# Kernel tuning notes

Measured on AMD Instinct MI355X. Metric: run time of the kernel, lower is better.

## Reference

```python
import jax, jax.numpy as jnp
import numpy as np

ALPHA = 0.2  # LeakyReLU negative slope
NEG_INF = -9e15  # matches torch's -9000000000000000.0


def setup_inputs() -> dict:
    key = jax.random.key(0)
    k1, k2, k3, k4 = jax.random.split(key, 4)
    B, T, N, F_in, D = 4, 32, 512, 128, 128
    h = jax.random.normal(k1, (B, T, N, F_in), dtype=jnp.float32)
    adj = jax.random.randint(k2, (N, N), 0, 2, dtype=jnp.int32)
    # params: W ~ Linear(in_dim, out_dim, bias=False); a ~ Linear(2*out_dim, 1, bias=False)
    W = jax.random.normal(k3, (F_in, D), dtype=jnp.float32) * 0.05
    a = jax.random.normal(k4, (2 * D,), dtype=jnp.float32) * 0.05
    return {"h": h, "adj": adj, "W": W, "a": a}


def reference(h, adj, W, a):
    # h: (B,T,N,F_in), adj: (N,N), W: (F_in,D), a: (2D,)
    D = W.shape[1]
    Wh = jnp.einsum('btnf,fd->btnd', h, W)  # (B,T,N,D)
    # a . [Wh_i ; Wh_j] == a_src . Wh_i + a_dst . Wh_j -- avoids (N,N,2D) concat
    a_src, a_dst = a[:D], a[D:]
    e_src = Wh @ a_src  # (B,T,N)
    e_dst = Wh @ a_dst  # (B,T,N)
    e = jax.nn.leaky_relu(e_src[..., :, None] + e_dst[..., None, :], ALPHA)  # (B,T,N,N)
    e = jnp.where(adj > 0, e, jnp.float32(NEG_INF))
    attention = jax.nn.softmax(e, axis=-1)  # dropout is identity at eval
    h_prime = jnp.einsum('btij,btjd->btid', attention, Wh)  # (B,T,N,D)
    return h_prime
```

## Files before the change

kernel.cpp:

```cpp
#include <hip/hip_runtime.h>
#include <math.h>

typedef __attribute__((ext_vector_type(8))) short bf16x8;
typedef __attribute__((ext_vector_type(4))) float f32x4;

#define MFMA(a, b, c) __builtin_amdgcn_mfma_f32_16x16x32_bf16(a, b, c, 0, 0, 0)

constexpr int GN = 128;
constexpr int NN = 512;
constexpr int FD = 128;
#define LOG2E 1.4426950408889634f

__device__ inline unsigned rne_top16(float x) {
    unsigned u = __float_as_uint(x);
    return u + 0x7fffu + ((u >> 16) & 1u);
}
__device__ inline unsigned pack_top16(unsigned e1, unsigned e0) {
    return __builtin_amdgcn_perm(e1, e0, 0x07060302u);
}

__global__ __launch_bounds__(512, 2) void gat_fused_kernel(
    const float* __restrict__ h, const float* __restrict__ a,
    const int* __restrict__ adj, const float* __restrict__ W,
    float* __restrict__ out)
{
    __shared__ __attribute__((aligned(16))) unsigned short sWh[65536];
    __shared__ __attribute__((aligned(16))) unsigned short sWc[8192];
    __shared__ __attribute__((aligned(16))) float sEsrc[NN];
    __shared__ __attribute__((aligned(16))) float sEdst[NN];

    const int bid = blockIdx.x;
    const int xcd = bid & 7, slot = bid >> 3;
    const int g  = xcd * 16 + (slot >> 1);
    const int hf = slot & 1;
    const int t = threadIdx.x, lane = t & 63, w = t >> 6;
    const int l15 = lane & 15, q8 = (lane >> 4) * 8;
    const float* hg = h + (size_t)g * NN * FD;

    f32x4 acc1[4][8];
    #pragma unroll
    for (int mt = 0; mt < 4; ++mt)
        #pragma unroll
        for (int nb = 0; nb < 8; ++nb) acc1[mt][nb] = (f32x4){0.f, 0.f, 0.f, 0.f};

    const int sd = w * 16 + l15;

    #pragma unroll
    for (int kk = 0; kk < 4; ++kk) {
        float4 hv[8];
        #pragma unroll
        for (int mt = 0; mt < 4; ++mt) {
            const float* src = hg + (size_t)(w * 64 + mt * 16 + l15) * FD
                             + kk * 32 + q8;
            hv[2 * mt]     = *(const float4*)src;
            hv[2 * mt + 1] = *(const float4*)(src + 4);
        }

        if (kk > 0) __syncthreads();
        {
            const int kbase = kk * 32 + q8;
            unsigned hi[8], lo[8];
            #pragma unroll
            for (int idx = 0; idx < 8; ++idx) {
                const float wv = W[(kbase + idx) * FD + sd];
                const unsigned u = __float_as_uint(wv);
                hi[idx] = u;
                lo[idx] = rne_top16(wv - __uint_as_float(u & 0xffff0000u));
            }
            uint4 H4, L4;
            H4.x = pack_top16(hi[1], hi[0]); H4.y = pack_top16(hi[3], hi[2]);
            H4.z = pack_top16(hi[5], hi[4]); H4.w = pack_top16(hi[7], hi[6]);
            L4.x = pack_top16(lo[1], lo[0]); L4.y = pack_top16(lo[3], lo[2]);
            L4.z = pack_top16(lo[5], lo[4]); L4.w = pack_top16(lo[7], lo[6]);
            *(uint4*)&sWc[t * 8]        = H4;
            *(uint4*)&sWc[4096 + t * 8] = L4;
        }
        __syncthreads();

        bf16x8 ah[4], al[4];
        #pragma unroll
        for (int mt = 0; mt < 4; ++mt) {
            const float4 f0 = hv[2 * mt], f1 = hv[2 * mt + 1];
            const float xs[8] = {f0.x, f0.y, f0.z, f0.w, f1.x, f1.y, f1.z, f1.w};
            union { bf16x8 v; unsigned u[4]; } H, L;
            #pragma unroll
            for (int j = 0; j < 4; ++j) {
                const unsigned e0 = __float_as_uint(xs[2 * j]);
                const unsigned e1 = __float_as_uint(xs[2 * j + 1]);
                H.u[j] = pack_top16(e1, e0);
                const unsigned l0 = rne_top16(xs[2*j]   - __uint_as_float(e0 & 0xffff0000u));
                const unsigned l1 = rne_top16(xs[2*j+1] - __uint_as_float(e1 & 0xffff0000u));
                L.u[j] = pack_top16(l1, l0);
            }
            ah[mt] = H.v; al[mt] = L.v;
        }
        #pragma unroll
        for (int nb = 0; nb < 8; ++nb) {
            const bf16x8 bh = *(const bf16x8*)&sWc[(nb * 64 + lane) * 8];
            const bf16x8 bl = *(const bf16x8*)&sWc[4096 + (nb * 64 + lane) * 8];
            #pragma unroll
            for (int mt = 0; mt < 4; ++mt) {
                acc1[mt][nb] = MFMA(al[mt], bh, acc1[mt][nb]);
                acc1[mt][nb] = MFMA(ah[mt], bl, acc1[mt][nb]);
                acc1[mt][nb] = MFMA(ah[mt], bh, acc1[mt][nb]);
            }
        }
    }

    {
        float av[8], bv[8];
        #pragma unroll
        for (int nb = 0; nb < 8; ++nb) {
            av[nb] = a[nb * 16 + l15];
            bv[nb] = a[FD + nb * 16 + l15];
        }
        #pragma unroll
        for (int mt = 0; mt < 4; ++mt)
            #pragma unroll
            for (int r = 0; r < 4; ++r) {
                float ps = 0.f, pd = 0.f;
                #pragma unroll
                for (int nb = 0; nb < 8; ++nb) {
                    ps += acc1[mt][nb][r] * av[nb];
                    pd += acc1[mt][nb][r] * bv[nb];
                }
                #pragma unroll
                for (int off = 1; off <= 8; off <<= 1) {
                    ps += __shfl_xor(ps, off);
                    pd += __shfl_xor(pd, off);
                }
                if (l15 == 0) {
                    const int row = w * 64 + mt * 16 + (lane >> 4) * 4 + r;
                    sEsrc[row] = ps * LOG2E;
                    sEdst[row] = pd * LOG2E;
                }
            }
    }

    {
        const int ib = 4 * ((lane >> 4) & 1);
        #pragma unroll
        for (int mt = 0; mt < 4; ++mt) {
            const int KK = w * 2 + (mt >> 1);
            const int lp2 = l15 + 16 * ((mt & 1) * 2 + (lane >> 5));
            #pragma unroll
            for (int nb = 0; nb < 8; ++nb) {
                const int off = ((KK * 8 + nb) * 64 + lp2) * 8 + ib;
                const unsigned r0 = rne_top16(acc1[mt][nb][0]);
                const unsigned r1 = rne_top16(acc1[mt][nb][1]);
                const unsigned r2 = rne_top16(acc1[mt][nb][2]);
                const unsigned r3 = rne_top16(acc1[mt][nb][3]);
                *(uint2*)&sWh[off] = make_uint2(pack_top16(r1, r0), pack_top16(r3, r2));
            }
        }
    }
    __syncthreads();

    const int rloc0 = w * 32 + l15;
    const int irow0 = hf * 256 + rloc0;
    const int irow1 = irow0 + 16;
    const float s0 = sEsrc[irow0];
    const float s1 = sEsrc[irow1];
    const int* adjr0 = adj + (size_t)irow0 * NN;
    const int* adjr1 = adj + (size_t)irow1 * NN;

    union { bf16x8 v; unsigned short s[8]; } bo;
    {
        const unsigned short oneb = (l15 == 0) ? (unsigned short)0x3f80 : (unsigned short)0;
        #pragma unroll
        for (int j = 0; j < 8; ++j) bo.s[j] = oneb;
    }

    f32x4 acc[2][8];
    #pragma unroll
    for (int mt = 0; mt < 2; ++mt)
        #pragma unroll
        for (int nb = 0; nb < 8; ++nb) acc[mt][nb] = (f32x4){0.f, 0.f, 0.f, 0.f};
    f32x4 accS0 = (f32x4){0.f, 0.f, 0.f, 0.f};
    f32x4 accS1 = (f32x4){0.f, 0.f, 0.f, 0.f};

    int4 n00 = *(const int4*)&adjr0[q8];
    int4 n01 = *(const int4*)&adjr0[q8 + 4];
    int4 n10 = *(const int4*)&adjr1[q8];
    int4 n11 = *(const int4*)&adjr1[q8 + 4];

    for (int KK = 0; KK < 16; ++KK) {
        const int4 m00 = n00, m01 = n01, m10 = n10, m11 = n11;
        if (KK < 15) {
            const int jb = (KK + 1) * 32 + q8;
            n00 = *(const int4*)&adjr0[jb];
            n01 = *(const int4*)&adjr0[jb + 4];
            n10 = *(const int4*)&adjr1[jb];
            n11 = *(const int4*)&adjr1[jb + 4];
        }
        const float* ep = &sEdst[KK * 32 + q8];
        const float4 ed0 = *(const float4*)ep;
        const float4 ed1 = *(const float4*)(ep + 4);
        const float ev[8] = {ed0.x, ed0.y, ed0.z, ed0.w, ed1.x, ed1.y, ed1.z, ed1.w};
        int ma0[8], ma1[8];
        *(int4*)&ma0[0] = m00; *(int4*)&ma0[4] = m01;
        *(int4*)&ma1[0] = m10; *(int4*)&ma1[4] = m11;

        union { bf16x8 v; unsigned u[4]; } H0, H1;
        unsigned uh0[8], uh1[8];
        #pragma unroll
        for (int i = 0; i < 8; ++i) {
            const float z0 = s0 + ev[i];
            float p0 = __builtin_amdgcn_exp2f(fmaxf(z0, 0.2f * z0));
            p0 = (ma0[i] > 0) ? p0 : 0.f;
            uh0[i] = __float_as_uint(p0);
            const float z1 = s1 + ev[i];
            float p1 = __builtin_amdgcn_exp2f(fmaxf(z1, 0.2f * z1));
            p1 = (ma1[i] > 0) ? p1 : 0.f;
            uh1[i] = __float_as_uint(p1);
        }
        #pragma unroll
        for (int j = 0; j < 4; ++j) {
            H0.u[j] = pack_top16(uh0[2*j+1], uh0[2*j]);
            H1.u[j] = pack_top16(uh1[2*j+1], uh1[2*j]);
        }
        #pragma unroll
        for (int nb = 0; nb < 8; ++nb) {
            const bf16x8 bh = *(const bf16x8*)&sWh[((KK * 8 + nb) * 64 + lane) * 8];
            acc[0][nb] = MFMA(H0.v, bh, acc[0][nb]);
            acc[1][nb] = MFMA(H1.v, bh, acc[1][nb]);
        }
        accS0 = MFMA(H0.v, bo.v, accS0);
        accS1 = MFMA(H1.v, bo.v, accS1);
    }

    #pragma unroll
    for (int r = 0; r < 4; ++r) {
        const float rl0 = 1.0f / __shfl(accS0[r], lane & 48);
        const float rl1 = 1.0f / __shfl(accS1[r], lane & 48);
        const int row0 = g * NN + hf * 256 + w * 32 + (lane >> 4) * 4 + r;
        const int row1 = row0 + 16;
        #pragma unroll
        for (int nb = 0; nb < 8; ++nb) {
            out[row0 * FD + nb * 16 + l15] = acc[0][nb][r] * rl0;
            out[row1 * FD + nb * 16 + l15] = acc[1][nb][r] * rl1;
        }
    }
}

extern "C" void kernel_launch(void* const* d_in, const int* in_sizes, int n_in,
                              void* d_out, int out_size, void* d_ws, size_t ws_size,
                              hipStream_t stream) {
    const float* h   = (const float*)d_in[0];
    const int*   adj = (const int*)d_in[1];
    const float* W   = (const float*)d_in[2];
    const float* a   = (const float*)d_in[3];
    float* out = (float*)d_out;
    (void)d_ws; (void)ws_size;

    gat_fused_kernel<<<256, 512, 0, stream>>>(h, a, adj, W, out);
}
```

Measured before the change: 117.4 us.

## Double block to 1024 threads, split attention K-range across wave pairs

Launches 1024-thread blocks (16 waves) instead of 512. Each wave now computes 32 rows of Wh instead of 64, and W is converted to split bf16 once into the (not yet used) upper half of sWh instead of being restaged per k-slice, which removes the per-slice barriers. In the attention phase, pairs of waves split the 16 key chunks in half, and partial outputs and row sums are reduced through shared memory before the normalised store. This adds two barriers and an LDS reduction, and at 1024 threads each wave has a smaller register budget, in exchange for more waves per CU to hide latency.

```diff
diff --git a/kernel.cpp b/kernel.cpp
--- a/kernel.cpp
+++ b/kernel.cpp
@@ -19,13 +19,12 @@
     return __builtin_amdgcn_perm(e1, e0, 0x07060302u);
 }
 
-__global__ __launch_bounds__(512, 2) void gat_fused_kernel(
+__global__ __launch_bounds__(1024) void gat_fused_kernel(
     const float* __restrict__ h, const float* __restrict__ a,
     const int* __restrict__ adj, const float* __restrict__ W,
     float* __restrict__ out)
 {
     __shared__ __attribute__((aligned(16))) unsigned short sWh[65536];
-    __shared__ __attribute__((aligned(16))) unsigned short sWc[8192];
     __shared__ __attribute__((aligned(16))) float sEsrc[NN];
     __shared__ __attribute__((aligned(16))) float sEdst[NN];
 
@@ -37,49 +36,49 @@
     const int l15 = lane & 15, q8 = (lane >> 4) * 8;
     const float* hg = h + (size_t)g * NN * FD;
 
-    f32x4 acc1[4][8];
-    #pragma unroll
-    for (int mt = 0; mt < 4; ++mt)
+    #pragma unroll
+    for (int rep = 0; rep < 2; ++rep) {
+        const int p = rep * 1024 + t;
+        const int lanep = p & 63, cn2 = p >> 6;
+        const int kbase = (cn2 >> 3) * 32 + ((lanep >> 4) & 3) * 8;
+        const int d = (cn2 & 7) * 16 + (lanep & 15);
+        unsigned hi[8], lo[8];
+        #pragma unroll
+        for (int idx = 0; idx < 8; ++idx) {
+            const float wv = W[(kbase + idx) * FD + d];
+            const unsigned u = __float_as_uint(wv);
+            hi[idx] = u;
+            lo[idx] = rne_top16(wv - __uint_as_float(u & 0xffff0000u));
+        }
+        uint4 H4, L4;
+        H4.x = pack_top16(hi[1], hi[0]); H4.y = pack_top16(hi[3], hi[2]);
+        H4.z = pack_top16(hi[5], hi[4]); H4.w = pack_top16(hi[7], hi[6]);
+        L4.x = pack_top16(lo[1], lo[0]); L4.y = pack_top16(lo[3], lo[2]);
+        L4.z = pack_top16(lo[5], lo[4]); L4.w = pack_top16(lo[7], lo[6]);
+        *(uint4*)&sWh[32768 + p * 8] = H4;
+        *(uint4*)&sWh[49152 + p * 8] = L4;
+    }
+    __syncthreads();
+
+    f32x4 acc1[2][8];
+    #pragma unroll
+    for (int mt = 0; mt < 2; ++mt)
         #pragma unroll
         for (int nb = 0; nb < 8; ++nb) acc1[mt][nb] = (f32x4){0.f, 0.f, 0.f, 0.f};
 
-    const int sd = w * 16 + l15;
-
     #pragma unroll
     for (int kk = 0; kk < 4; ++kk) {
-        float4 hv[8];
-        #pragma unroll
-        for (int mt = 0; mt < 4; ++mt) {
-            const float* src = hg + (size_t)(w * 64 + mt * 16 + l15) * FD
+        float4 hv[4];
+        #pragma unroll
+        for (int mt = 0; mt < 2; ++mt) {
+            const float* src = hg + (size_t)(w * 32 + mt * 16 + l15) * FD
                              + kk * 32 + q8;
             hv[2 * mt]     = *(const float4*)src;
             hv[2 * mt + 1] = *(const float4*)(src + 4);
         }
-
-        if (kk > 0) __syncthreads();
-        {
-            const int kbase = kk * 32 + q8;
-            unsigned hi[8], lo[8];
-            #pragma unroll
-            for (int idx = 0; idx < 8; ++idx) {
-                const float wv = W[(kbase + idx) * FD + sd];
-                const unsigned u = __float_as_uint(wv);
-                hi[idx] = u;
-                lo[idx] = rne_top16(wv - __uint_as_float(u & 0xffff0000u));
-            }
-            uint4 H4, L4;
-            H4.x = pack_top16(hi[1], hi[0]); H4.y = pack_top16(hi[3], hi[2]);
-            H4.z = pack_top16(hi[5], hi[4]); H4.w = pack_top16(hi[7], hi[6]);
-            L4.x = pack_top16(lo[1], lo[0]); L4.y = pack_top16(lo[3], lo[2]);
-            L4.z = pack_top16(lo[5], lo[4]); L4.w = pack_top16(lo[7], lo[6]);
-            *(uint4*)&sWc[t * 8]        = H4;
-            *(uint4*)&sWc[4096 + t * 8] = L4;
-        }
-        __syncthreads();
-
-        bf16x8 ah[4], al[4];
-        #pragma unroll
-        for (int mt = 0; mt < 4; ++mt) {
+        bf16x8 ah[2], al[2];
+        #pragma unroll
+        for (int mt = 0; mt < 2; ++mt) {
             const float4 f0 = hv[2 * mt], f1 = hv[2 * mt + 1];
             const float xs[8] = {f0.x, f0.y, f0.z, f0.w, f1.x, f1.y, f1.z, f1.w};
             union { bf16x8 v; unsigned u[4]; } H, L;
@@ -96,10 +95,10 @@
         }
         #pragma unroll
         for (int nb = 0; nb < 8; ++nb) {
-            const bf16x8 bh = *(const bf16x8*)&sWc[(nb * 64 + lane) * 8];
-            const bf16x8 bl = *(const bf16x8*)&sWc[4096 + (nb * 64 + lane) * 8];
-            #pragma unroll
-            for (int mt = 0; mt < 4; ++mt) {
+            const bf16x8 bh = *(const bf16x8*)&sWh[32768 + ((kk * 8 + nb) * 64 + lane) * 8];
+            const bf16x8 bl = *(const bf16x8*)&sWh[49152 + ((kk * 8 + nb) * 64 + lane) * 8];
+            #pragma unroll
+            for (int mt = 0; mt < 2; ++mt) {
                 acc1[mt][nb] = MFMA(al[mt], bh, acc1[mt][nb]);
                 acc1[mt][nb] = MFMA(ah[mt], bl, acc1[mt][nb]);
                 acc1[mt][nb] = MFMA(ah[mt], bh, acc1[mt][nb]);
@@ -115,7 +114,7 @@
             bv[nb] = a[FD + nb * 16 + l15];
         }
         #pragma unroll
-        for (int mt = 0; mt < 4; ++mt)
+        for (int mt = 0; mt < 2; ++mt)
             #pragma unroll
             for (int r = 0; r < 4; ++r) {
                 float ps = 0.f, pd = 0.f;
@@ -130,22 +129,22 @@
                     pd += __shfl_xor(pd, off);
                 }
                 if (l15 == 0) {
-                    const int row = w * 64 + mt * 16 + (lane >> 4) * 4 + r;
+                    const int row = w * 32 + mt * 16 + (lane >> 4) * 4 + r;
                     sEsrc[row] = ps * LOG2E;
                     sEdst[row] = pd * LOG2E;
                 }
             }
     }
+    __syncthreads();
 
     {
         const int ib = 4 * ((lane >> 4) & 1);
         #pragma unroll
-        for (int mt = 0; mt < 4; ++mt) {
-            const int KK = w * 2 + (mt >> 1);
-            const int lp2 = l15 + 16 * ((mt & 1) * 2 + (lane >> 5));
+        for (int mt = 0; mt < 2; ++mt) {
+            const int lp2 = l15 + 16 * (mt * 2 + (lane >> 5));
             #pragma unroll
             for (int nb = 0; nb < 8; ++nb) {
-                const int off = ((KK * 8 + nb) * 64 + lp2) * 8 + ib;
+                const int off = ((w * 8 + nb) * 64 + lp2) * 8 + ib;
                 const unsigned r0 = rne_top16(acc1[mt][nb][0]);
                 const unsigned r1 = rne_top16(acc1[mt][nb][1]);
                 const unsigned r2 = rne_top16(acc1[mt][nb][2]);
@@ -156,7 +155,8 @@
     }
     __syncthreads();
 
-    const int rloc0 = w * 32 + l15;
+    const int rg = w >> 1, jh = w & 1;
+    const int rloc0 = rg * 32 + l15;
     const int irow0 = hf * 256 + rloc0;
     const int irow1 = irow0 + 16;
     const float s0 = sEsrc[irow0];
@@ -179,14 +179,16 @@
     f32x4 accS0 = (f32x4){0.f, 0.f, 0.f, 0.f};
     f32x4 accS1 = (f32x4){0.f, 0.f, 0.f, 0.f};
 
-    int4 n00 = *(const int4*)&adjr0[q8];
-    int4 n01 = *(const int4*)&adjr0[q8 + 4];
-    int4 n10 = *(const int4*)&adjr1[q8];
-    int4 n11 = *(const int4*)&adjr1[q8 + 4];
-
-    for (int KK = 0; KK < 16; ++KK) {
+    const int k0 = jh * 8;
+    int4 n00 = *(const int4*)&adjr0[k0 * 32 + q8];
+    int4 n01 = *(const int4*)&adjr0[k0 * 32 + q8 + 4];
+    int4 n10 = *(const int4*)&adjr1[k0 * 32 + q8];
+    int4 n11 = *(const int4*)&adjr1[k0 * 32 + q8 + 4];
+
+    for (int kl = 0; kl < 8; ++kl) {
+        const int KK = k0 + kl;
         const int4 m00 = n00, m01 = n01, m10 = n10, m11 = n11;
-        if (KK < 15) {
+        if (kl < 7) {
             const int jb = (KK + 1) * 32 + q8;
             n00 = *(const int4*)&adjr0[jb];
             n01 = *(const int4*)&adjr0[jb + 4];
@@ -229,16 +231,47 @@
         accS1 = MFMA(H1.v, bo.v, accS1);
     }
 
-    #pragma unroll
-    for (int r = 0; r < 4; ++r) {
-        const float rl0 = 1.0f / __shfl(accS0[r], lane & 48);
-        const float rl1 = 1.0f / __shfl(accS1[r], lane & 48);
-        const int row0 = g * NN + hf * 256 + w * 32 + (lane >> 4) * 4 + r;
-        const int row1 = row0 + 16;
-        #pragma unroll
-        for (int nb = 0; nb < 8; ++nb) {
-            out[row0 * FD + nb * 16 + l15] = acc[0][nb][r] * rl0;
-            out[row1 * FD + nb * 16 + l15] = acc[1][nb][r] * rl1;
+    __syncthreads();
+
+    float* sPartF = (float*)sWh;
+    if (jh == 1) {
+        #pragma unroll
+        for (int mt = 0; mt < 2; ++mt)
+            #pragma unroll
+            for (int nb = 0; nb < 8; ++nb)
+                *(f32x4*)&sPartF[(((rg * 2 + mt) * 8 + nb) * 64 + lane) * 4] = acc[mt][nb];
+        if (l15 == 0) {
+            #pragma unroll
+            for (int r = 0; r < 4; ++r) {
+                sEsrc[rg * 32 + (lane >> 4) * 4 + r]      = accS0[r];
+                sEsrc[rg * 32 + 16 + (lane >> 4) * 4 + r] = accS1[r];
+            }
+        }
+    }
+    __syncthreads();
+
+    if (jh == 0) {
+        #pragma unroll
+        for (int mt = 0; mt < 2; ++mt)
+            #pragma unroll
+            for (int nb = 0; nb < 8; ++nb) {
+                const f32x4 p = *(const f32x4*)&sPartF[(((rg * 2 + mt) * 8 + nb) * 64 + lane) * 4];
+                acc[mt][nb][0] += p[0]; acc[mt][nb][1] += p[1];
+                acc[mt][nb][2] += p[2]; acc[mt][nb][3] += p[3];
+            }
+        #pragma unroll
+        for (int r = 0; r < 4; ++r) {
+            const float rl0 = 1.0f / (__shfl(accS0[r], lane & 48)
+                                      + sEsrc[rg * 32 + (lane >> 4) * 4 + r]);
+            const float rl1 = 1.0f / (__shfl(accS1[r], lane & 48)
+                                      + sEsrc[rg * 32 + 16 + (lane >> 4) * 4 + r]);
+            const int row0 = g * NN + hf * 256 + rg * 32 + (lane >> 4) * 4 + r;
+            const int row1 = row0 + 16;
+            #pragma unroll
+            for (int nb = 0; nb < 8; ++nb) {
+                out[row0 * FD + nb * 16 + l15] = acc[0][nb][r] * rl0;
+                out[row1 * FD + nb * 16 + l15] = acc[1][nb][r] * rl1;
+            }
         }
     }
 }
@@ -253,5 +286,5 @@
     float* out = (float*)d_out;
     (void)d_ws; (void)ws_size;
 
-    gat_fused_kernel<<<256, 512, 0, stream>>>(h, a, adj, W, out);
-}
+    gat_fused_kernel<<<256, 1024, 0, stream>>>(h, a, adj, W, out);
+}
```

Measured after the change: 116.9 us. No clear change (-0.4%).
